# Performance work log

Hardware: AMD Instinct MI355X
Metric: run time of the kernel (lower is better)

The kernel has to match this reference:

```python
import jax, jax.numpy as jnp
import numpy as np
from jax import lax

B, CI, CO, H, W = 8, 128, 256, 56, 56
P, K = 9, 3  # num_paths, kernel_size


def setup_inputs() -> dict:
    key = jax.random.key(0)
    ks = jax.random.split(key, 7)
    s_conv = 1.0 / np.sqrt(CI * K * K)
    s_o1 = 1.0 / np.sqrt(CI)
    s_o2 = 1.0 / np.sqrt(CO // 2)
    return {
        "x": jax.random.normal(ks[0], (B, CI, H, W), dtype=jnp.float32),
        # num_paths independent 3x3 convs, stacked on leading axis
        "kw": jax.random.uniform(ks[1], (P, CO, CI, K, K), jnp.float32, -s_conv, s_conv),
        "kb": jax.random.uniform(ks[2], (P, CO), jnp.float32, -s_conv, s_conv),
        # observer: 1x1 conv CI -> CO//2, tanh, 1x1 conv CO//2 -> P
        "ow1": jax.random.uniform(ks[3], (CO // 2, CI), jnp.float32, -s_o1, s_o1),
        "ob1": jax.random.uniform(ks[4], (CO // 2,), jnp.float32, -s_o1, s_o1),
        "ow2": jax.random.uniform(ks[5], (P, CO // 2), jnp.float32, -s_o2, s_o2),
        "ob2": jax.random.uniform(ks[6], (P,), jnp.float32, -s_o2, s_o2),
    }


def reference(x, kw, kb, ow1, ob1, ow2, ob2):
    p, co, ci, k, _ = kw.shape
    b, _, h, w = x.shape
    # All num_paths convs as a single grouped-output conv: (P*CO, CI, K, K)
    wflat = kw.reshape(p * co, ci, k, k)
    paths = lax.conv_general_dilated(
        x, wflat, window_strides=(1, 1), padding=((1, 1), (1, 1)),
        dimension_numbers=("NCHW", "OIHW", "NCHW"))
    paths = paths + kb.reshape(p * co)[None, :, None, None]
    paths = paths.reshape(b, p, co, h, w)  # [B,P,CO,H,W]

    # observer: two 1x1 convs (pure channel mixes) with tanh in between
    hmid = jnp.tanh(jnp.einsum("bchw,dc->bdhw", x, ow1) + ob1[None, :, None, None])
    scores = jnp.einsum("bdhw,pd->bphw", hmid, ow2) + ob2[None, :, None, None]

    # eval-mode collapse: argmax over paths, pixel-wise hard selection.
    # (one-hot multiply + sum over paths == gather of the winning path)
    idx = jnp.argmax(scores, axis=1)  # [B,H,W]
    out = jnp.take_along_axis(paths, idx[:, None, None, :, :], axis=1)[:, 0]  # [B,CO,H,W]
    return jax.nn.relu(out)  # norm_type='none' -> identity norm
```

## Files before the change

### kernel.cpp

```cpp
#include <hip/hip_runtime.h>
#include <hip/hip_bf16.h>


typedef unsigned int u32;

#define NPIX    25088
#define OFF_LIST 4096
#define OFF_XPAD 907264
#define OFF_W2   7796736
#define OFF_P2R  13105152
#define OFF_OUTC 13205504

__device__ __forceinline__ unsigned short f2bf(float f) {
  u32 u = __builtin_bit_cast(u32, f);
  u32 r = (u + 0x7FFFu + ((u >> 16) & 1u)) >> 16;
  return (unsigned short)r;
}
__device__ __forceinline__ float bflo(u32 w) {
  return __builtin_bit_cast(float, w << 16);
}
__device__ __forceinline__ float bfhi(u32 w) {
  return __builtin_bit_cast(float, w & 0xFFFF0000u);
}

#define GLDS16(g, l)                                                        \
  __builtin_amdgcn_global_load_lds(                                         \
      (const __attribute__((address_space(1))) u32*)(g),                    \
      (__attribute__((address_space(3))) u32*)(l), 16, 0, 0)

typedef __attribute__((ext_vector_type(8))) short bf16x8;
typedef __attribute__((ext_vector_type(4))) float f32x4;

__global__ __launch_bounds__(512) void k_front(
    const float* __restrict__ x, const float* __restrict__ kw,
    const float* __restrict__ ow1, const float* __restrict__ ob1,
    const float* __restrict__ ow2, const float* __restrict__ ob2,
    u32* __restrict__ xpad, u32* __restrict__ w2,
    int* __restrict__ cnt, int* __restrict__ list) {
  __shared__ float red[8][64][9];
  __shared__ int lcnt[9], lbase[9];

  int bid = blockIdx.x;
  int tid = threadIdx.x;

  if (bid < 392) {
    int px = tid & 63;
    int dg = tid >> 6;
    int dgu = __builtin_amdgcn_readfirstlane(dg);
    int pix = bid * 64 + px;
    int b = pix / 3136, s = pix - b * 3136;
    const float* xb = x + (size_t)b * 401408 + s;

    if (tid < 9) lcnt[tid] = 0;

    float h[16];
    const float* o1 = ob1 + dgu * 16;
#pragma unroll
    for (int i = 0; i < 16; ++i) h[i] = o1[i];

    const float* w1b = ow1 + dgu * 16 * 128;
    for (int cc = 0; cc < 128; cc += 8) {
      float xc[8];
#pragma unroll
      for (int j = 0; j < 8; ++j) xc[j] = xb[(size_t)(cc + j) * 3136];
#pragma unroll
      for (int i = 0; i < 16; ++i) {
        const float* wr = w1b + i * 128 + cc;
        float a = h[i];
#pragma unroll
        for (int j = 0; j < 8; ++j) a = fmaf(wr[j], xc[j], a);
        h[i] = a;
      }
    }

#pragma unroll
    for (int i = 0; i < 16; ++i) h[i] = tanhf(h[i]);

#pragma unroll
    for (int p = 0; p < 9; ++p) {
      float sc = 0.f;
      const float* wr = ow2 + p * 128 + dgu * 16;
#pragma unroll
      for (int i = 0; i < 16; ++i) sc = fmaf(wr[i], h[i], sc);
      red[dg][px][p] = sc;
    }
    __syncthreads();

    int bi = 0, slot = 0;
    if (dg == 0) {
      float best = 0.f;
#pragma unroll
      for (int p = 0; p < 9; ++p) {
        float v = ob2[p];
#pragma unroll
        for (int g = 0; g < 8; ++g) v += red[g][px][p];
        if (p == 0 || v > best) { best = v; bi = p; }
      }
      slot = atomicAdd(&lcnt[bi], 1);
    }
    __syncthreads();
    if (tid < 9) lbase[tid] = atomicAdd(&cnt[tid], lcnt[tid]);
    __syncthreads();
    if (dg == 0) list[bi * NPIX + lbase[bi] + slot] = pix;

  } else if (bid < 840) {
    int bh = bid - 392;
    int b = bh / 56, hh = bh - b * 56;
    int cp = tid & 63;
    int wq = tid >> 6;
    const float* xb = x + (size_t)(b * 128 + 2 * cp) * 3136 + hh * 56;
    u32* orow = xpad + (size_t)(b * 58 + hh + 1) * 58 * 64;
    for (int w = wq; w < 56; w += 8) {
      float f0 = xb[w];
      float f1 = xb[3136 + w];
      orow[(w + 1) * 64 + cp] = (u32)f2bf(f0) | ((u32)f2bf(f1) << 16);
    }
    if (wq == 0) orow[cp] = 0;
    else if (wq == 1) orow[57 * 64 + cp] = 0;

  } else if (bid < 856) {
    int r = bid - 840;
    int b = r >> 1;
    u32* orow = xpad + ((size_t)(b * 58) + ((r & 1) ? 57 : 0)) * 58 * 64;
    for (int i = tid; i < 58 * 64; i += 512) orow[i] = 0;

  } else {
    for (int t = (bid - 856) * 512 + tid; t < 1327104; t += 256 * 512) {
      int cp = t & 63;
      int r = t >> 6;
      int tap = r % 9;
      int pco = r / 9;
      const float* sp = kw + ((size_t)pco * 128 + 2 * cp) * 9 + tap;
      w2[t] = (u32)f2bf(sp[0]) | ((u32)f2bf(sp[9]) << 16);
    }
  }
}

__global__ __launch_bounds__(256, 4) void k_conv(
    const int* __restrict__ cnt, const int* __restrict__ list,
    const char* __restrict__ xpadB, const char* __restrict__ w2B,
    const float* __restrict__ kb, unsigned short* __restrict__ outcH,
    int* __restrict__ pix2row) {
  __shared__ short Wlds[2][4096];
  __shared__ short Plds[2][2048];
  __shared__ int offsB[64];
  __shared__ float kbl[128];

  int bid = blockIdx.x;
  int half = bid & 1, tb = bid >> 1;
  int p = -1, cntp = 0, baseP = 0, accb = 0;
  for (int pp = 0; pp < 9; ++pp) {
    int c = cnt[pp];
    int tt = (c + 63) >> 6;
    if (p < 0) {
      if (tb < tt) { p = pp; cntp = c; baseP = accb; }
      else tb -= tt;
    }
    accb += c;
  }
  if (p < 0) return;
  int nbase = tb * 64;
  int tid = threadIdx.x;

  if (tid < 64) {
    int g = nbase + tid;
    bool v = g < cntp;
    int pixid = list[p * NPIX + (v ? g : nbase)];
    int b = pixid / 3136, s = pixid - b * 3136;
    int h = s / 56, w = s - h * 56;
    offsB[tid] = ((b * 58 + h) * 58 + w) * 256;
    if (v && half == 0) pix2row[pixid] = baseP + g;
  }
  if (tid < 128) kbl[tid] = kb[p * 256 + half * 128 + tid];
  __syncthreads();

  int segsw = ((tid & 3) ^ ((tid >> 3) & 3)) * 16;
  int na = tid >> 2;
  int offP = offsB[na] + segsw;
  const char* wrow = w2B + (size_t)(p * 256 + half * 128) * 2304;
  const char* wp0 = wrow + (size_t)na * 2304 + segsw;
  const char* wp1 = wrow + (size_t)(64 + na) * 2304 + segsw;

  auto stage = [&](int c, int q) {
    int tap = c >> 2, kc = c & 3;
    int wko = tap * 256 + kc * 64;
    int tapoff = ((tap / 3) * 58 + (tap % 3)) * 256 + kc * 64;
    GLDS16(wp0 + wko, &Wlds[q][tid * 8]);
    GLDS16(wp1 + wko, &Wlds[q][2048 + tid * 8]);
    GLDS16(xpadB + (size_t)(offP + tapoff), &Plds[q][tid * 8]);
  };

  f32x4 acc[4][2];
#pragma unroll
  for (int mt = 0; mt < 4; ++mt)
#pragma unroll
    for (int nt = 0; nt < 2; ++nt) acc[mt][nt] = (f32x4)0.f;

  int lane = tid & 63, wave = tid >> 6;
  int wm = wave >> 1, wn = wave & 1;
  int l15 = lane & 15, quad = lane >> 4;
  int slot = (quad ^ ((l15 >> 1) & 3)) * 8;
  int mrow = wm * 64 + l15;
  int nrow = wn * 32 + l15;

  stage(0, 0);
  for (int c = 0; c < 36; ++c) {
    __syncthreads();
    if (c + 1 < 36) stage(c + 1, (c + 1) & 1);
    int q = c & 1;
    bf16x8 af[4], bfr[2];
#pragma unroll
    for (int mt = 0; mt < 4; ++mt)
      af[mt] = *(const bf16x8*)&Wlds[q][(mrow + mt * 16) * 32 + slot];
#pragma unroll
    for (int nt = 0; nt < 2; ++nt)
      bfr[nt] = *(const bf16x8*)&Plds[q][(nrow + nt * 16) * 32 + slot];
#pragma unroll
    for (int mt = 0; mt < 4; ++mt)
#pragma unroll
      for (int nt = 0; nt < 2; ++nt)
        acc[mt][nt] = __builtin_amdgcn_mfma_f32_16x16x32_bf16(
            af[mt], bfr[nt], acc[mt][nt], 0, 0, 0);
  }

#pragma unroll
  for (int nt = 0; nt < 2; ++nt) {
    int n = wn * 32 + nt * 16 + l15;
    if ((nbase + n) >= cntp) continue;
    size_t rowb = (size_t)(baseP + nbase + n) * 256 + half * 128;
#pragma unroll
    for (int mt = 0; mt < 4; ++mt) {
      int co0 = wm * 64 + mt * 16 + quad * 4;
      float v0 = acc[mt][nt][0] + kbl[co0 + 0];
      float v1 = acc[mt][nt][1] + kbl[co0 + 1];
      float v2 = acc[mt][nt][2] + kbl[co0 + 2];
      float v3 = acc[mt][nt][3] + kbl[co0 + 3];
      v0 = v0 > 0.f ? v0 : 0.f;  v1 = v1 > 0.f ? v1 : 0.f;
      v2 = v2 > 0.f ? v2 : 0.f;  v3 = v3 > 0.f ? v3 : 0.f;
      u32 lo = (u32)f2bf(v0) | ((u32)f2bf(v1) << 16);
      u32 hi = (u32)f2bf(v2) | ((u32)f2bf(v3) << 16);
      *(u32*)&outcH[rowb + co0]     = lo;
      *(u32*)&outcH[rowb + co0 + 2] = hi;
    }
  }
}

__global__ __launch_bounds__(256) void k_out(
    const int* __restrict__ pix2row, const u32* __restrict__ outcU,
    float* __restrict__ out) {
  int tid = threadIdx.x;
  int pl = tid & 63, coq = tid >> 6;
  int pix = blockIdx.x * 64 + pl;
  int b = pix / 3136, s = pix - b * 3136;
  int row = pix2row[pix];
  const u32* src = outcU + (size_t)row * 128 + coq * 32;
  float* dst = out + (size_t)b * 802816 + s;
#pragma unroll
  for (int j = 0; j < 8; ++j) {
    uint4 w = *(const uint4*)(src + j * 4);
    int co = coq * 64 + j * 8;
    dst[(size_t)(co + 0) * 3136] = bflo(w.x);
    dst[(size_t)(co + 1) * 3136] = bfhi(w.x);
    dst[(size_t)(co + 2) * 3136] = bflo(w.y);
    dst[(size_t)(co + 3) * 3136] = bfhi(w.y);
    dst[(size_t)(co + 4) * 3136] = bflo(w.z);
    dst[(size_t)(co + 5) * 3136] = bfhi(w.z);
    dst[(size_t)(co + 6) * 3136] = bflo(w.w);
    dst[(size_t)(co + 7) * 3136] = bfhi(w.w);
  }
}

extern "C" void kernel_launch(void* const* d_in, const int* in_sizes, int n_in,
                              void* d_out, int out_size, void* d_ws, size_t ws_size,
                              hipStream_t stream) {
  const float* x   = (const float*)d_in[0];
  const float* kw  = (const float*)d_in[1];
  const float* kb  = (const float*)d_in[2];
  const float* ow1 = (const float*)d_in[3];
  const float* ob1 = (const float*)d_in[4];
  const float* ow2 = (const float*)d_in[5];
  const float* ob2 = (const float*)d_in[6];
  float* out = (float*)d_out;
  char* ws = (char*)d_ws;

  int* cnt  = (int*)(ws);
  int* list = (int*)(ws + OFF_LIST);
  u32* xpad = (u32*)(ws + OFF_XPAD);
  u32* w2   = (u32*)(ws + OFF_W2);
  int* p2r  = (int*)(ws + OFF_P2R);
  unsigned short* outc = (unsigned short*)(ws + OFF_OUTC);

  hipMemsetAsync(cnt, 0, 64, stream);

  k_front<<<1112, 512, 0, stream>>>(x, kw, ow1, ob1, ow2, ob2, xpad, w2,
                                    cnt, list);
  k_conv<<<802, 256, 0, stream>>>(cnt, list, (const char*)xpad, (const char*)w2,
                                  kb, outc, p2r);
  k_out<<<392, 256, 0, stream>>>(p2r, (const u32*)outc, out);
}
```

Before: 165.4 us.

## Restructure front kernel: LDS-staged transposes, coalesced loads, prefetch, 256-thread blocks

Moves the front kernel to 256-thread blocks. Each observer wave now computes 32 hidden units and prefetches the next channel chunk of x. The x-to-bf16 padded transpose and the weight repack both go through shared memory, so global reads and writes are coalesced instead of strided. The halo-row zeroing is folded into the row blocks for hh==0 and hh==55. The aim is to cut uncoalesced memory traffic in the preprocessing stage, at the cost of more registers per thread in the observer path and extra block synchronisation.

```diff
diff --git a/kernel.cpp b/kernel.cpp
--- a/kernel.cpp
+++ b/kernel.cpp
@@ -31,40 +31,51 @@
 typedef __attribute__((ext_vector_type(8))) short bf16x8;
 typedef __attribute__((ext_vector_type(4))) float f32x4;
 
-__global__ __launch_bounds__(512) void k_front(
+__global__ __launch_bounds__(256) void k_front(
     const float* __restrict__ x, const float* __restrict__ kw,
     const float* __restrict__ ow1, const float* __restrict__ ob1,
     const float* __restrict__ ow2, const float* __restrict__ ob2,
     u32* __restrict__ xpad, u32* __restrict__ w2,
     int* __restrict__ cnt, int* __restrict__ list) {
-  __shared__ float red[8][64][9];
-  __shared__ int lcnt[9], lbase[9];
+  __shared__ union {
+    struct {
+      float red[4][64][9];
+      int lcnt[9], lbase[9];
+    } o;
+    u32 xt[56 * 65];
+    float kt[2 * 1152];
+  } sm;
 
   int bid = blockIdx.x;
   int tid = threadIdx.x;
+  int ln = tid & 63, wv = tid >> 6;
 
   if (bid < 392) {
-    int px = tid & 63;
-    int dg = tid >> 6;
-    int dgu = __builtin_amdgcn_readfirstlane(dg);
-    int pix = bid * 64 + px;
+    int dgu = __builtin_amdgcn_readfirstlane(wv);
+    int pix = bid * 64 + ln;
     int b = pix / 3136, s = pix - b * 3136;
     const float* xb = x + (size_t)b * 401408 + s;
 
-    if (tid < 9) lcnt[tid] = 0;
-
-    float h[16];
-    const float* o1 = ob1 + dgu * 16;
-#pragma unroll
-    for (int i = 0; i < 16; ++i) h[i] = o1[i];
-
-    const float* w1b = ow1 + dgu * 16 * 128;
+    if (tid < 9) sm.o.lcnt[tid] = 0;
+
+    float h[32];
+    const float* o1 = ob1 + dgu * 32;
+#pragma unroll
+    for (int i = 0; i < 32; ++i) h[i] = o1[i];
+
+    const float* w1b = ow1 + dgu * 32 * 128;
+    float xc[8], xn[8];
+#pragma unroll
+    for (int j = 0; j < 8; ++j) xn[j] = xb[(size_t)j * 3136];
     for (int cc = 0; cc < 128; cc += 8) {
-      float xc[8];
-#pragma unroll
-      for (int j = 0; j < 8; ++j) xc[j] = xb[(size_t)(cc + j) * 3136];
-#pragma unroll
-      for (int i = 0; i < 16; ++i) {
+#pragma unroll
+      for (int j = 0; j < 8; ++j) xc[j] = xn[j];
+      if (cc + 8 < 128) {
+#pragma unroll
+        for (int j = 0; j < 8; ++j) xn[j] = xb[(size_t)(cc + 8 + j) * 3136];
+      }
+#pragma unroll
+      for (int i = 0; i < 32; ++i) {
         const float* wr = w1b + i * 128 + cc;
         float a = h[i];
 #pragma unroll
@@ -74,64 +85,76 @@
     }
 
 #pragma unroll
-    for (int i = 0; i < 16; ++i) h[i] = tanhf(h[i]);
+    for (int i = 0; i < 32; ++i) h[i] = tanhf(h[i]);
 
 #pragma unroll
     for (int p = 0; p < 9; ++p) {
       float sc = 0.f;
-      const float* wr = ow2 + p * 128 + dgu * 16;
-#pragma unroll
-      for (int i = 0; i < 16; ++i) sc = fmaf(wr[i], h[i], sc);
-      red[dg][px][p] = sc;
+      const float* wr = ow2 + p * 128 + dgu * 32;
+#pragma unroll
+      for (int i = 0; i < 32; ++i) sc = fmaf(wr[i], h[i], sc);
+      sm.o.red[wv][ln][p] = sc;
     }
     __syncthreads();
 
     int bi = 0, slot = 0;
-    if (dg == 0) {
+    if (wv == 0) {
       float best = 0.f;
 #pragma unroll
       for (int p = 0; p < 9; ++p) {
         float v = ob2[p];
 #pragma unroll
-        for (int g = 0; g < 8; ++g) v += red[g][px][p];
+        for (int g = 0; g < 4; ++g) v += sm.o.red[g][ln][p];
         if (p == 0 || v > best) { best = v; bi = p; }
       }
-      slot = atomicAdd(&lcnt[bi], 1);
-    }
-    __syncthreads();
-    if (tid < 9) lbase[tid] = atomicAdd(&cnt[tid], lcnt[tid]);
-    __syncthreads();
-    if (dg == 0) list[bi * NPIX + lbase[bi] + slot] = pix;
+      slot = atomicAdd(&sm.o.lcnt[bi], 1);
+    }
+    __syncthreads();
+    if (tid < 9) sm.o.lbase[tid] = atomicAdd(&cnt[tid], sm.o.lcnt[tid]);
+    __syncthreads();
+    if (wv == 0) list[bi * NPIX + sm.o.lbase[bi] + slot] = pix;
 
   } else if (bid < 840) {
     int bh = bid - 392;
     int b = bh / 56, hh = bh - b * 56;
-    int cp = tid & 63;
-    int wq = tid >> 6;
-    const float* xb = x + (size_t)(b * 128 + 2 * cp) * 3136 + hh * 56;
+    const float* xr = x + (size_t)b * 401408 + hh * 56;
+#pragma unroll
+    for (int r = 0; r < 16; ++r) {
+      int ci = wv * 32 + 2 * r;
+      if (ln < 56) {
+        float f0 = xr[(size_t)ci * 3136 + ln];
+        float f1 = xr[(size_t)(ci + 1) * 3136 + ln];
+        sm.xt[ln * 65 + (ci >> 1)] = (u32)f2bf(f0) | ((u32)f2bf(f1) << 16);
+      }
+    }
+    __syncthreads();
     u32* orow = xpad + (size_t)(b * 58 + hh + 1) * 58 * 64;
-    for (int w = wq; w < 56; w += 8) {
-      float f0 = xb[w];
-      float f1 = xb[3136 + w];
-      orow[(w + 1) * 64 + cp] = (u32)f2bf(f0) | ((u32)f2bf(f1) << 16);
-    }
-    if (wq == 0) orow[cp] = 0;
-    else if (wq == 1) orow[57 * 64 + cp] = 0;
-
-  } else if (bid < 856) {
-    int r = bid - 840;
-    int b = r >> 1;
-    u32* orow = xpad + ((size_t)(b * 58) + ((r & 1) ? 57 : 0)) * 58 * 64;
-    for (int i = tid; i < 58 * 64; i += 512) orow[i] = 0;
+    for (int w = wv; w < 56; w += 4)
+      orow[(w + 1) * 64 + ln] = sm.xt[w * 65 + ln];
+    if (wv == 0) orow[ln] = 0;
+    else if (wv == 1) orow[57 * 64 + ln] = 0;
+    if (hh == 0) {
+      u32* hrow = xpad + (size_t)(b * 58) * 58 * 64;
+      for (int i = tid; i < 58 * 64; i += 256) hrow[i] = 0;
+    } else if (hh == 55) {
+      u32* hrow = xpad + (size_t)(b * 58 + 57) * 58 * 64;
+      for (int i = tid; i < 58 * 64; i += 256) hrow[i] = 0;
+    }
 
   } else {
-    for (int t = (bid - 856) * 512 + tid; t < 1327104; t += 256 * 512) {
-      int cp = t & 63;
-      int r = t >> 6;
-      int tap = r % 9;
-      int pco = r / 9;
-      const float* sp = kw + ((size_t)pco * 128 + 2 * cp) * 9 + tap;
-      w2[t] = (u32)f2bf(sp[0]) | ((u32)f2bf(sp[9]) << 16);
+    int base = (bid - 840) * 2;
+    const float* src = kw + (size_t)base * 1152;
+#pragma unroll
+    for (int i = 0; i < 9; ++i) sm.kt[i * 256 + tid] = src[i * 256 + tid];
+    __syncthreads();
+#pragma unroll
+    for (int pl = 0; pl < 2; ++pl) {
+      for (int d = tid; d < 576; d += 256) {
+        int tap = d >> 6, cp = d & 63;
+        float v0 = sm.kt[pl * 1152 + (2 * cp) * 9 + tap];
+        float v1 = sm.kt[pl * 1152 + (2 * cp + 1) * 9 + tap];
+        w2[(size_t)(base + pl) * 576 + d] = (u32)f2bf(v0) | ((u32)f2bf(v1) << 16);
+      }
     }
   }
 }
@@ -292,7 +315,7 @@
 
   hipMemsetAsync(cnt, 0, 64, stream);
 
-  k_front<<<1112, 512, 0, stream>>>(x, kw, ow1, ob1, ow2, ob2, xpad, w2,
+  k_front<<<1992, 256, 0, stream>>>(x, kw, ow1, ob1, ow2, ob2, xpad, w2,
                                     cnt, list);
   k_conv<<<802, 256, 0, stream>>>(cnt, list, (const char*)xpad, (const char*)w2,
                                   kb, outc, p2r);
```

Result: slower. 174.6 us (+5.5%).

## Coalesce front-kernel loads via LDS staging and transposes for observer, xpad and weights

Applied to the files above, without the earlier changes.

The observer branch now loads x channel chunks into LDS with double-buffered global_load_lds, so each wave no longer re-reads the same x values, and the reduction buffer shares that LDS. The x-to-padded-bf16 conversion now reads rows coalesced and transposes through padded LDS, and the halo-row zeroing is folded into the first and last row blocks. The weight repack now stages contiguous kw blocks in LDS before transposing, which needs more blocks (grid grows to 1416). This adds extra syncs and LDS use per block in exchange for coalesced global accesses.

```diff
diff --git a/kernel.cpp b/kernel.cpp
--- a/kernel.cpp
+++ b/kernel.cpp
@@ -27,6 +27,10 @@
   __builtin_amdgcn_global_load_lds(                                         \
       (const __attribute__((address_space(1))) u32*)(g),                    \
       (__attribute__((address_space(3))) u32*)(l), 16, 0, 0)
+#define GLDS4(g, l)                                                         \
+  __builtin_amdgcn_global_load_lds(                                         \
+      (const __attribute__((address_space(1))) u32*)(g),                    \
+      (__attribute__((address_space(3))) u32*)(l), 4, 0, 0)
 
 typedef __attribute__((ext_vector_type(8))) short bf16x8;
 typedef __attribute__((ext_vector_type(4))) float f32x4;
@@ -37,19 +41,21 @@
     const float* __restrict__ ow2, const float* __restrict__ ob2,
     u32* __restrict__ xpad, u32* __restrict__ w2,
     int* __restrict__ cnt, int* __restrict__ list) {
-  __shared__ float red[8][64][9];
+  __shared__ __attribute__((aligned(16))) char smraw[18432];
   __shared__ int lcnt[9], lbase[9];
 
   int bid = blockIdx.x;
   int tid = threadIdx.x;
+  int ln = tid & 63, wv = tid >> 6;
 
   if (bid < 392) {
-    int px = tid & 63;
-    int dg = tid >> 6;
-    int dgu = __builtin_amdgcn_readfirstlane(dg);
-    int pix = bid * 64 + px;
-    int b = pix / 3136, s = pix - b * 3136;
-    const float* xb = x + (size_t)b * 401408 + s;
+    float* xlds = (float*)smraw;
+    float* red  = (float*)smraw;
+    int dgu = __builtin_amdgcn_readfirstlane(wv);
+    int pix0 = bid * 64;
+    int b = pix0 / 3136, s0 = pix0 - b * 3136;
+    int pix = pix0 + ln;
+    const float* xsrc = x + (size_t)b * 401408 + s0 + ln;
 
     if (tid < 9) lcnt[tid] = 0;
 
@@ -57,12 +63,21 @@
     const float* o1 = ob1 + dgu * 16;
 #pragma unroll
     for (int i = 0; i < 16; ++i) h[i] = o1[i];
-
     const float* w1b = ow1 + dgu * 16 * 128;
-    for (int cc = 0; cc < 128; cc += 8) {
+
+    auto stage = [&](int c, int q) {
+      GLDS4(xsrc + (size_t)(8 * c + wv) * 3136, &xlds[q * 512 + wv * 64 + ln]);
+    };
+
+    stage(0, 0);
+    for (int c = 0; c < 16; ++c) {
+      __syncthreads();
+      if (c + 1 < 16) stage(c + 1, (c + 1) & 1);
+      const float* xq = &xlds[(c & 1) * 512];
       float xc[8];
 #pragma unroll
-      for (int j = 0; j < 8; ++j) xc[j] = xb[(size_t)(cc + j) * 3136];
+      for (int j = 0; j < 8; ++j) xc[j] = xq[j * 64 + ln];
+      int cc = c * 8;
 #pragma unroll
       for (int i = 0; i < 16; ++i) {
         const float* wr = w1b + i * 128 + cc;
@@ -72,6 +87,7 @@
         h[i] = a;
       }
     }
+    __syncthreads();
 
 #pragma unroll
     for (int i = 0; i < 16; ++i) h[i] = tanhf(h[i]);
@@ -82,18 +98,18 @@
       const float* wr = ow2 + p * 128 + dgu * 16;
 #pragma unroll
       for (int i = 0; i < 16; ++i) sc = fmaf(wr[i], h[i], sc);
-      red[dg][px][p] = sc;
+      red[wv * 576 + ln * 9 + p] = sc;
     }
     __syncthreads();
 
     int bi = 0, slot = 0;
-    if (dg == 0) {
+    if (wv == 0) {
       float best = 0.f;
 #pragma unroll
       for (int p = 0; p < 9; ++p) {
         float v = ob2[p];
 #pragma unroll
-        for (int g = 0; g < 8; ++g) v += red[g][px][p];
+        for (int g = 0; g < 8; ++g) v += red[g * 576 + ln * 9 + p];
         if (p == 0 || v > best) { best = v; bi = p; }
       }
       slot = atomicAdd(&lcnt[bi], 1);
@@ -101,37 +117,49 @@
     __syncthreads();
     if (tid < 9) lbase[tid] = atomicAdd(&cnt[tid], lcnt[tid]);
     __syncthreads();
-    if (dg == 0) list[bi * NPIX + lbase[bi] + slot] = pix;
+    if (wv == 0) list[bi * NPIX + lbase[bi] + slot] = pix;
 
   } else if (bid < 840) {
+    u32* xt = (u32*)smraw;
     int bh = bid - 392;
     int b = bh / 56, hh = bh - b * 56;
-    int cp = tid & 63;
-    int wq = tid >> 6;
-    const float* xb = x + (size_t)(b * 128 + 2 * cp) * 3136 + hh * 56;
+    const float* xr = x + (size_t)b * 401408 + hh * 56;
+#pragma unroll
+    for (int r = 0; r < 8; ++r) {
+      int ci = wv * 16 + 2 * r;
+      if (ln < 56) {
+        float f0 = xr[(size_t)ci * 3136 + ln];
+        float f1 = xr[(size_t)(ci + 1) * 3136 + ln];
+        xt[ln * 65 + (ci >> 1)] = (u32)f2bf(f0) | ((u32)f2bf(f1) << 16);
+      }
+    }
+    __syncthreads();
     u32* orow = xpad + (size_t)(b * 58 + hh + 1) * 58 * 64;
-    for (int w = wq; w < 56; w += 8) {
-      float f0 = xb[w];
-      float f1 = xb[3136 + w];
-      orow[(w + 1) * 64 + cp] = (u32)f2bf(f0) | ((u32)f2bf(f1) << 16);
-    }
-    if (wq == 0) orow[cp] = 0;
-    else if (wq == 1) orow[57 * 64 + cp] = 0;
-
-  } else if (bid < 856) {
-    int r = bid - 840;
-    int b = r >> 1;
-    u32* orow = xpad + ((size_t)(b * 58) + ((r & 1) ? 57 : 0)) * 58 * 64;
-    for (int i = tid; i < 58 * 64; i += 512) orow[i] = 0;
+    for (int w = wv; w < 56; w += 8)
+      orow[(w + 1) * 64 + ln] = xt[w * 65 + ln];
+    if (wv == 0) orow[ln] = 0;
+    else if (wv == 1) orow[57 * 64 + ln] = 0;
+    if (hh == 0) {
+      u32* hrow = xpad + (size_t)(b * 58) * 58 * 64;
+      for (int i = tid; i < 58 * 64; i += 512) hrow[i] = 0;
+    } else if (hh == 55) {
+      u32* hrow = xpad + (size_t)(b * 58 + 57) * 58 * 64;
+      for (int i = tid; i < 58 * 64; i += 512) hrow[i] = 0;
+    }
 
   } else {
-    for (int t = (bid - 856) * 512 + tid; t < 1327104; t += 256 * 512) {
-      int cp = t & 63;
-      int r = t >> 6;
-      int tap = r % 9;
-      int pco = r / 9;
-      const float* sp = kw + ((size_t)pco * 128 + 2 * cp) * 9 + tap;
-      w2[t] = (u32)f2bf(sp[0]) | ((u32)f2bf(sp[9]) << 16);
+    float* kt = (float*)smraw;
+    int base = (bid - 840) * 4;
+    const float* src = kw + (size_t)base * 1152;
+#pragma unroll
+    for (int i = 0; i < 9; ++i) kt[i * 512 + tid] = src[i * 512 + tid];
+    __syncthreads();
+    for (int t = tid; t < 2304; t += 512) {
+      int pl = t / 576, d = t - pl * 576;
+      int tap = d >> 6, cp = d & 63;
+      float v0 = kt[pl * 1152 + 18 * cp + tap];
+      float v1 = kt[pl * 1152 + 18 * cp + 9 + tap];
+      w2[(size_t)(base + pl) * 576 + d] = (u32)f2bf(v0) | ((u32)f2bf(v1) << 16);
     }
   }
 }
@@ -292,7 +320,7 @@
 
   hipMemsetAsync(cnt, 0, 64, stream);
 
-  k_front<<<1112, 512, 0, stream>>>(x, kw, ow1, ob1, ow2, ob2, xpad, w2,
+  k_front<<<1416, 512, 0, stream>>>(x, kw, ow1, ob1, ow2, ob2, xpad, w2,
                                     cnt, list);
   k_conv<<<802, 256, 0, stream>>>(cnt, list, (const char*)xpad, (const char*)w2,
                                   kb, outc, p2r);
```

Result: no change. 164.0 us (-0.9%).
